# Optimization experiments

Hardware: AMD Instinct MI355X
Metric: run time of the kernel (lower is better)

## Reference

```python
import jax, jax.numpy as jnp
import numpy as np

GRID_SIZE = 10
SPLINE_ORDER = 3
GRID_RANGE = (0.0, 1.0)
COUNT_HARMONIC = 8


def make_grid():
    # knot vector: (grid_size + 2*spline_order + 1,) = (17,), same for every input feature
    h = (GRID_RANGE[1] - GRID_RANGE[0]) / GRID_SIZE
    return (jnp.arange(-SPLINE_ORDER, GRID_SIZE + SPLINE_ORDER + 1, dtype=jnp.float32) * h
            + GRID_RANGE[0])


def b_splines(x, grid):
    # x: (B, in) -> bases: (B, in, grid_size + spline_order) via Cox-de Boor recursion
    xg = x[..., None]                                   # (B, in, 1)
    bases = ((xg >= grid[:-1]) & (xg < grid[1:])).astype(x.dtype)  # (B, in, 16)
    for k in range(1, SPLINE_ORDER + 1):
        left = (xg - grid[:-(k + 1)]) / (grid[k:-1] - grid[:-(k + 1)]) * bases[..., :-1]
        right = (grid[k + 1:] - xg) / (grid[k + 1:] - grid[1:-k]) * bases[..., 1:]
        bases = left + right
    return bases                                        # (B, in, 13)


def kan_linear(x, base_w, spline_w, spline_scaler, grid):
    # base path: SiLU(x) @ W_base^T ; spline path: grouped weighted sum of B-spline bases
    base_out = jax.nn.silu(x) @ base_w.T                # (B, out)
    sp = b_splines(x, grid)                             # (B, in, C)
    sw = spline_w * spline_scaler[..., None]            # (out, in, C) standalone scaler
    spline_out = jnp.einsum('bic,oic->bo', sp, sw)
    return base_out + spline_out


def fft_calc(x):
    # x: (B, C, 64); two 32-sample windows, keep first count_harmonic+1 = 9 bins
    prev = jnp.fft.rfft(x[:, :, :32])[:, :, :COUNT_HARMONIC + 1]
    cur = jnp.fft.rfft(x[:, :, 32:])[:, :, :COUNT_HARMONIC + 1]
    # NOTE: original code uses the *current* window's phase twice (faithful to source)
    return jnp.concatenate(
        [jnp.abs(prev), jnp.angle(cur), jnp.abs(cur), jnp.angle(cur)], axis=-1)  # (B, C, 36)


def mlp_head(h, W1, b1, W2, b2, W3, b3):
    y = h @ W1.T + b1
    # nn.LeakyReLU(True) -> negative_slope = 1.0 -> identity (faithful to source)
    y = y @ W2.T + b2
    y = jnp.where(y >= 0, y, 0.05 * y)                  # LeakyReLU(0.05)
    y = y @ W3.T + b3
    return jax.nn.sigmoid(y)                            # (B, 1)


def setup_inputs() -> dict:
    key = jax.random.key(0)
    ks = jax.random.split(key, 20)
    B = 8192
    def n(i, shape):
        return jax.random.normal(ks[i], shape, dtype=jnp.float32)
    return {
        'x': n(0, (B, 64, 14)),
        'k1_base': n(1, (80, 504)), 'k1_spline': n(2, (80, 504, 13)), 'k1_scaler': n(3, (80, 504)),
        'k2_base': n(4, (160, 80)), 'k2_spline': n(5, (160, 80, 13)), 'k2_scaler': n(6, (160, 80)),
        'k3_base': n(7, (80, 160)), 'k3_spline': n(8, (80, 160, 13)), 'k3_scaler': n(9, (80, 160)),
        'k4_base': n(10, (40, 80)), 'k4_spline': n(11, (40, 80, 13)), 'k4_scaler': n(12, (40, 80)),
        'heads_W1': n(13, (3, 40, 40)), 'heads_b1': n(14, (3, 40)),
        'heads_W2': n(15, (3, 20, 40)), 'heads_b2': n(16, (3, 20)),
        'heads_W3': n(17, (3, 1, 20)), 'heads_b3': n(18, (3, 1)),
    }


def reference(x, k1_base, k1_spline, k1_scaler, k2_base, k2_spline, k2_scaler,
              k3_base, k3_spline, k3_scaler, k4_base, k4_spline, k4_scaler,
              heads_W1, heads_b1, heads_W2, heads_b2, heads_W3, heads_b3):
    B = x.shape[0]
    grid = make_grid()
    # original uses reshape (not transpose): (B, 64, 14) -> (B, 14, 64)
    h = x.reshape(B, x.shape[2], x.shape[1])
    h = fft_calc(h).reshape(B, -1)                      # (B, 504)
    h = kan_linear(h, k1_base, k1_spline, k1_scaler, grid)   # (B, 80)
    h = kan_linear(h, k2_base, k2_spline, k2_scaler, grid)   # (B, 160)
    h = kan_linear(h, k3_base, k3_spline, k3_scaler, grid)   # (B, 80)
    h = kan_linear(h, k4_base, k4_spline, k4_scaler, grid)   # (B, 40)
    heads = jax.vmap(lambda W1, b1, W2, b2, W3, b3: mlp_head(h, W1, b1, W2, b2, W3, b3))(
        heads_W1, heads_b1, heads_W2, heads_b2, heads_W3, heads_b3)  # (3, B, 1)
    return jnp.transpose(heads, (1, 0, 2)).reshape(B, 3)
```

## Files before the change

### kernel.cpp

```cpp
#include <hip/hip_runtime.h>
#include <math.h>


__device__ __forceinline__ float silu_f(float x) {
    return x / (1.f + __expf(-x));
}

__global__ __launch_bounds__(128) void fft_kernel(const float* __restrict__ x,
                                                  float* __restrict__ F0, int P) {
    __shared__ float xs[128 * 65];
    __shared__ float twc[288], tws[288];
    int tid = threadIdx.x;
    for (int t = tid; t < 288; t += 128) {
        int k = t >> 5, n = t & 31;
        int m = (k * n) & 31;
        float ang = -0.19634954084936207f * (float)m;
        float s, c;
        sincosf(ang, &s, &c);
        twc[t] = c; tws[t] = s;
    }
    int p0 = blockIdx.x * 128;
    for (int idx = tid; idx < 128 * 64; idx += 128) {
        int g = p0 * 64 + idx;
        float v = (g < P * 64) ? x[g] : 0.f;
        xs[(idx >> 6) * 65 + (idx & 63)] = v;
    }
    __syncthreads();
    int p = p0 + tid;
    if (p >= P) return;
    const float* row = &xs[tid * 65];
    float r[64];
#pragma unroll
    for (int n = 0; n < 64; ++n) r[n] = row[n];
    float outv[27];
#pragma unroll
    for (int k = 0; k < 9; ++k) {
        float rp = 0.f, ip = 0.f, rc = 0.f, ic = 0.f;
#pragma unroll
        for (int n = 0; n < 32; ++n) {
            float c = twc[k * 32 + n], s = tws[k * 32 + n];
            rp = fmaf(r[n], c, rp);
            ip = fmaf(r[n], s, ip);
            rc = fmaf(r[n + 32], c, rc);
            ic = fmaf(r[n + 32], s, ic);
        }
        float ap = sqrtf(fmaf(rp, rp, ip * ip));
        float ac = sqrtf(fmaf(rc, rc, ic * ic));
        float gc = atan2f(ic, rc);
        outv[k] = ap; outv[9 + k] = gc; outv[18 + k] = ac;
    }
    float* dst = &F0[(size_t)p * 27];
#pragma unroll
    for (int q = 0; q < 27; ++q) dst[q] = outv[q];
}

__global__ __launch_bounds__(256) void transpose_f0_kernel(const float* __restrict__ F0,
                                                           float* __restrict__ F0T, int B) {
    __shared__ float t[448 * 27];
    int b0 = blockIdx.x * 32;
    const float* src = F0 + (size_t)b0 * 14 * 27;
    for (int idx = threadIdx.x; idx < 448 * 27; idx += 256) t[idx] = src[idx];
    __syncthreads();
    for (int idx = threadIdx.x; idx < 378 * 32; idx += 256) {
        int i = idx >> 5, bb = idx & 31;
        int ch = i / 27, q = i - ch * 27;
        F0T[(size_t)i * B + b0 + bb] = t[(bb * 14 + ch) * 27 + q];
    }
}

__device__ __forceinline__ float kval(const float* __restrict__ bw,
                                      const float* __restrict__ sw,
                                      const float* __restrict__ sc,
                                      int IN, int o, int s, int c) {
    if (c == 0) return bw[o * IN + s];
    return sw[((size_t)o * IN + s) * 13 + (c - 1)] * sc[o * IN + s];
}

__global__ void prep_all_kernel(float* __restrict__ Wfp1, float* __restrict__ Wfp2,
                                float* __restrict__ Wfp3, float* __restrict__ Wfp4,
                                float* __restrict__ W21, float* __restrict__ b21,
                                const float* k1b, const float* k1s, const float* k1c,
                                const float* k2b, const float* k2s, const float* k2c,
                                const float* k3b, const float* k3s, const float* k3c,
                                const float* k4b, const float* k4s, const float* k4c,
                                const float* W1, const float* b1,
                                const float* W2, const float* b2) {
    const int T1 = 189 * 2688, T2 = 40 * 2 * 2688, T3 = 80 * 2688, T4 = 40 * 1344;
    int id = blockIdx.x * 256 + threadIdx.x;
    if (id < T1) {
        int jg = id / 2688, t = id % 2688;
        int kc = t / 96, t2 = t % 96, ct = t2 / 12, r = t2 % 12;
        int i = 2 * jg + kc / 14, c = kc % 14, o = ct * 10 + r;
        float v = 0.f;
        if (r < 10) {
            int ch = i / 27, q = i - ch * 27, s1 = ch * 36 + q;
            v = kval(k1b, k1s, k1c, 504, o, s1, c);
            if (q >= 9 && q < 18) v += kval(k1b, k1s, k1c, 504, o, s1 + 18, c);
        }
        Wfp1[id] = v; return;
    }
    id -= T1;
    if (id < T2) {
        int jg = id / (2 * 2688), rem = id % (2 * 2688), half = rem / 2688, t = rem % 2688;
        int kc = t / 96, t2 = t % 96, ct = t2 / 12, r = t2 % 12;
        int i = 2 * jg + kc / 14, c = kc % 14, o = half * 80 + ct * 10 + r;
        Wfp2[id] = (r < 10) ? kval(k2b, k2s, k2c, 80, o, i, c) : 0.f; return;
    }
    id -= T2;
    if (id < T3) {
        int jg = id / 2688, t = id % 2688;
        int kc = t / 96, t2 = t % 96, ct = t2 / 12, r = t2 % 12;
        int i = 2 * jg + kc / 14, c = kc % 14, o = ct * 10 + r;
        Wfp3[id] = (r < 10) ? kval(k3b, k3s, k3c, 160, o, i, c) : 0.f; return;
    }
    id -= T3;
    if (id < T4) {
        int jg = id / 1344, t = id % 1344;
        int kc = t / 48, t2 = t % 48, ct = t2 / 12, r = t2 % 12;
        int i = 2 * jg + kc / 14, c = kc % 14, o = ct * 10 + r;
        Wfp4[id] = (r < 10) ? kval(k4b, k4s, k4c, 80, o, i, c) : 0.f; return;
    }
    id -= T4;
    if (id < 3 * 20 * 40) {
        int k = id % 40, rem = id / 40, j = rem % 20, h = rem / 20;
        float a = 0.f;
        for (int m = 0; m < 40; ++m)
            a = fmaf(W2[(h * 20 + j) * 40 + m], W1[(h * 40 + m) * 40 + k], a);
        W21[id] = a;
    } else if (id < 3 * 20 * 40 + 60) {
        int t = id - 2400, j = t % 20, h = t / 20;
        float a = b2[h * 20 + j];
        for (int m = 0; m < 40; ++m)
            a = fmaf(W2[(h * 20 + j) * 40 + m], b1[h * 40 + m], a);
        b21[t] = a;
    }
}

template <int OUT_T, int KC, int NHALF>
__global__ __launch_bounds__(256) void kan5_kernel(const float* __restrict__ XT, int B,
                                                   const float* __restrict__ Wfp,
                                                   float* __restrict__ YpT, int OUTF) {
    constexpr int BM = 128;
    constexpr int NR = 10;
    constexpr int COLS_T = OUT_T / NR;
    constexpr int ROWS_T = 256 / COLS_T;
    constexpr int MR = BM / ROWS_T;
    constexpr int NW = 28 * COLS_T * 12;
    constexpr int NCH = KC / 2;
    constexpr int WSTG = (NW + 255) / 256;
    static_assert(COLS_T * NR == OUT_T, "cols");
    static_assert(ROWS_T * MR == BM, "rows");
    static_assert(KC % 2 == 0, "even KC");

    __shared__ float Ws[NW];
    __shared__ float Ft[28 * BM];

    const int tid = threadIdx.x;
    const int rt = tid % ROWS_T, ct = tid / ROWS_T;
    const int b0 = blockIdx.x * BM;
    const int s = blockIdx.y;
    const int half = blockIdx.z;
    const int ibase = s * KC;
    const int kk = tid >> 7;
    const int rr = tid & 127;

    float acc[MR][NR];
#pragma unroll
    for (int m = 0; m < MR; ++m)
#pragma unroll
        for (int n = 0; n < NR; ++n) acc[m][n] = 0.f;

    const size_t wbase0 = ((size_t)(ibase / 2) * NHALF + half) * NW;
    float wreg[WSTG];
#pragma unroll
    for (int u = 0; u < WSTG; ++u) {
        int t = tid + u * 256;
        wreg[u] = (t < NW) ? Wfp[wbase0 + t] : 0.f;
    }
    float xreg = XT[(size_t)(ibase + kk) * B + b0 + rr];

    for (int j = 0; j < NCH; ++j) {
        __syncthreads();
#pragma unroll
        for (int u = 0; u < WSTG; ++u) {
            int t = tid + u * 256;
            if (t < NW) Ws[t] = wreg[u];
        }
        {
            float xs = xreg;
            float* dst = &Ft[kk * 14 * BM + rr];
            dst[0] = silu_f(xs);
#pragma unroll
            for (int c = 1; c < 14; ++c) dst[c * BM] = 0.f;
            float t10 = (xs + 0.3f) * 10.f;
            if (t10 >= 0.f && t10 < 16.f) {
                int jj = (int)t10;
                float u = t10 - (float)jj;
                float u2 = u * u, u3 = u2 * u, v = 1.f - u;
                float B0 = v * v * v * (1.f / 6.f);
                float B1 = (3.f * u3 - 6.f * u2 + 4.f) * (1.f / 6.f);
                float B2 = (-3.f * u3 + 3.f * u2 + 3.f * u + 1.f) * (1.f / 6.f);
                float B3 = u3 * (1.f / 6.f);
                int bs = jj - 3;
#pragma unroll
                for (int t = 0; t < 4; ++t) {
                    int rw = bs + t;
                    float bb = (t == 0) ? B0 : (t == 1) ? B1 : (t == 2) ? B2 : B3;
                    if (rw >= 0 && rw <= 12) dst[(1 + rw) * BM] = bb;
                }
            }
        }
        if (j + 1 < NCH) {
            const size_t wb = wbase0 + (size_t)(j + 1) * NHALF * NW;
#pragma unroll
            for (int u = 0; u < WSTG; ++u) {
                int t = tid + u * 256;
                if (t < NW) wreg[u] = Wfp[wb + t];
            }
            xreg = XT[(size_t)(ibase + 2 * (j + 1) + kk) * B + b0 + rr];
        }
        __syncthreads();
#pragma unroll
        for (int kc = 0; kc < 28; ++kc) {
            const float* wb = &Ws[(kc * COLS_T + ct) * 12];
            float4 w0 = *(const float4*)(wb);
            float4 w1 = *(const float4*)(wb + 4);
            float2 w2 = *(const float2*)(wb + 8);
            float wn[NR] = {w0.x, w0.y, w0.z, w0.w, w1.x, w1.y, w1.z, w1.w, w2.x, w2.y};
            const float* fb = &Ft[kc * BM + rt * MR];
            float xm[MR];
            if constexpr (MR == 4) {
                float4 f = *(const float4*)fb;
                xm[0] = f.x; xm[1] = f.y; xm[2] = f.z; xm[3] = f.w;
            } else {
                float2 f = *(const float2*)fb;
                xm[0] = f.x; xm[1] = f.y;
            }
#pragma unroll
            for (int m = 0; m < MR; ++m)
#pragma unroll
                for (int n = 0; n < NR; ++n) acc[m][n] = fmaf(xm[m], wn[n], acc[m][n]);
        }
    }

    float* yd = YpT + (size_t)s * OUTF * B + (size_t)(half * OUT_T) * B;
#pragma unroll
    for (int n = 0; n < NR; ++n) {
        float* p = yd + (size_t)(ct * NR + n) * B + b0 + rt * MR;
        if constexpr (MR == 4)
            *(float4*)p = make_float4(acc[0][n], acc[1][n], acc[2][n], acc[3][n]);
        else
            *(float2*)p = make_float2(acc[0][n], acc[1][n]);
    }
}

__global__ void reduce_kernel(float* __restrict__ Y, const float* __restrict__ Yp,
                              int N, int KS) {
    int t = blockIdx.x * 256 + threadIdx.x;
    if (t >= N) return;
    float a = 0.f;
    for (int s = 0; s < KS; ++s) a += Yp[(size_t)s * N + t];
    Y[t] = a;
}

__global__ __launch_bounds__(256) void heads_kernel(const float* __restrict__ h4T,
                                                    const float* __restrict__ W21,
                                                    const float* __restrict__ b21,
                                                    const float* __restrict__ W3,
                                                    const float* __restrict__ b3,
                                                    float* __restrict__ out, int B) {
    __shared__ float w21s[2400], b21s[60], w3s[60], b3s[3];
    int tid = threadIdx.x;
    for (int t = tid; t < 2400; t += 256) w21s[t] = W21[t];
    if (tid < 60) { b21s[tid] = b21[tid]; w3s[tid] = W3[tid]; }
    if (tid < 3) b3s[tid] = b3[tid];
    __syncthreads();
    int id = blockIdx.x * 256 + tid;
    if (id >= B * 3) return;
    int b = id / 3, h = id % 3;
    float hv[40];
#pragma unroll
    for (int m = 0; m < 40; ++m) hv[m] = h4T[(size_t)m * B + b];
    float z = b3s[h];
#pragma unroll
    for (int j = 0; j < 20; ++j) {
        float y = b21s[h * 20 + j];
        const float* wr = &w21s[(h * 20 + j) * 40];
#pragma unroll
        for (int m = 0; m < 40; ++m) y = fmaf(wr[m], hv[m], y);
        y = (y >= 0.f) ? y : 0.05f * y;
        z = fmaf(w3s[h * 20 + j], y, z);
    }
    out[id] = 1.f / (1.f + __expf(-z));
}

extern "C" void kernel_launch(void* const* d_in, const int* in_sizes, int n_in,
                              void* d_out, int out_size, void* d_ws, size_t ws_size,
                              hipStream_t stream) {
    const float* x   = (const float*)d_in[0];
    const float* k1b = (const float*)d_in[1];
    const float* k1s = (const float*)d_in[2];
    const float* k1c = (const float*)d_in[3];
    const float* k2b = (const float*)d_in[4];
    const float* k2s = (const float*)d_in[5];
    const float* k2c = (const float*)d_in[6];
    const float* k3b = (const float*)d_in[7];
    const float* k3s = (const float*)d_in[8];
    const float* k3c = (const float*)d_in[9];
    const float* k4b = (const float*)d_in[10];
    const float* k4s = (const float*)d_in[11];
    const float* k4c = (const float*)d_in[12];
    const float* hW1 = (const float*)d_in[13];
    const float* hb1 = (const float*)d_in[14];
    const float* hW2 = (const float*)d_in[15];
    const float* hb2 = (const float*)d_in[16];
    const float* hW3 = (const float*)d_in[17];
    const float* hb3 = (const float*)d_in[18];
    float* out = (float*)d_out;

    int B = in_sizes[0] / (64 * 14);
    int P = B * 14;

    float* ws = (float*)d_ws;
    size_t off = 0;
    float* Wfp1 = ws + off; off += 189 * 2688;
    float* Wfp2 = ws + off; off += 40 * 2 * 2688;
    float* Wfp3 = ws + off; off += 80 * 2688;
    float* Wfp4 = ws + off; off += 40 * 1344;
    float* W21  = ws + off; off += 2400;
    float* b21  = ws + off; off += 60;
    float* F0T  = ws + off; off += (size_t)B * 378;
    float* h1T  = ws + off; off += (size_t)B * 80;
    float* h2T  = ws + off; off += (size_t)B * 160;
    float* h3T  = ws + off; off += (size_t)B * 80;
    float* h4T  = ws + off; off += (size_t)B * 40;
    float* F0   = ws + off;
    float* Yp   = ws + off;
    size_t cap = (ws_size / 4 > off) ? (ws_size / 4 - off) : 0;
    int S1 = (cap >= (size_t)21 * B * 80) ? 21 : (cap >= (size_t)9 * B * 80) ? 9
           : (cap >= (size_t)7 * B * 80) ? 7 : 3;
    int S2 = (cap >= (size_t)10 * B * 160) ? 10 : (cap >= (size_t)5 * B * 160) ? 5 : 2;
    int S3 = (cap >= (size_t)20 * B * 80) ? 20 : (cap >= (size_t)8 * B * 80) ? 8 : 4;
    int S4 = (cap >= (size_t)10 * B * 40) ? 10 : 2;

    {
        int total = 189 * 2688 + 40 * 2 * 2688 + 80 * 2688 + 40 * 1344 + 2460;
        prep_all_kernel<<<(total + 255) / 256, 256, 0, stream>>>(
            Wfp1, Wfp2, Wfp3, Wfp4, W21, b21,
            k1b, k1s, k1c, k2b, k2s, k2c, k3b, k3s, k3c, k4b, k4s, k4c,
            hW1, hb1, hW2, hb2);
    }

    fft_kernel<<<(P + 127) / 128, 128, 0, stream>>>(x, F0, P);
    transpose_f0_kernel<<<B / 32, 256, 0, stream>>>(F0, F0T, B);

    if (S1 == 21)     kan5_kernel<80, 18, 1><<<dim3(B / 128, 21, 1), 256, 0, stream>>>(F0T, B, Wfp1, Yp, 80);
    else if (S1 == 9) kan5_kernel<80, 42, 1><<<dim3(B / 128, 9, 1), 256, 0, stream>>>(F0T, B, Wfp1, Yp, 80);
    else if (S1 == 7) kan5_kernel<80, 54, 1><<<dim3(B / 128, 7, 1), 256, 0, stream>>>(F0T, B, Wfp1, Yp, 80);
    else              kan5_kernel<80, 126, 1><<<dim3(B / 128, 3, 1), 256, 0, stream>>>(F0T, B, Wfp1, Yp, 80);
    reduce_kernel<<<((B * 80) + 255) / 256, 256, 0, stream>>>(h1T, Yp, B * 80, S1);

    if (S2 == 10)     kan5_kernel<80, 8, 2><<<dim3(B / 128, 10, 2), 256, 0, stream>>>(h1T, B, Wfp2, Yp, 160);
    else if (S2 == 5) kan5_kernel<80, 16, 2><<<dim3(B / 128, 5, 2), 256, 0, stream>>>(h1T, B, Wfp2, Yp, 160);
    else              kan5_kernel<80, 40, 2><<<dim3(B / 128, 2, 2), 256, 0, stream>>>(h1T, B, Wfp2, Yp, 160);
    reduce_kernel<<<((B * 160) + 255) / 256, 256, 0, stream>>>(h2T, Yp, B * 160, S2);

    if (S3 == 20)     kan5_kernel<80, 8, 1><<<dim3(B / 128, 20, 1), 256, 0, stream>>>(h2T, B, Wfp3, Yp, 80);
    else if (S3 == 8) kan5_kernel<80, 20, 1><<<dim3(B / 128, 8, 1), 256, 0, stream>>>(h2T, B, Wfp3, Yp, 80);
    else              kan5_kernel<80, 40, 1><<<dim3(B / 128, 4, 1), 256, 0, stream>>>(h2T, B, Wfp3, Yp, 80);
    reduce_kernel<<<((B * 80) + 255) / 256, 256, 0, stream>>>(h3T, Yp, B * 80, S3);

    if (S4 == 10) kan5_kernel<40, 8, 1><<<dim3(B / 128, 10, 1), 256, 0, stream>>>(h3T, B, Wfp4, Yp, 40);
    else          kan5_kernel<40, 40, 1><<<dim3(B / 128, 2, 1), 256, 0, stream>>>(h3T, B, Wfp4, Yp, 40);
    reduce_kernel<<<((B * 40) + 255) / 256, 256, 0, stream>>>(h4T, Yp, B * 40, S4);

    heads_kernel<<<(B * 3 + 255) / 256, 256, 0, stream>>>(h4T, W21, b21, hW3, hb3, out, B);

    (void)n_in; (void)out_size;
}
```

Baseline: 389.2 us.

## Double-buffer KAN shared tiles, vectorize split-K reduce, retune split counts

```diff
diff --git a/kernel.cpp b/kernel.cpp
--- a/kernel.cpp
+++ b/kernel.cpp
@@ -137,7 +137,7 @@
 }
 
 template <int OUT_T, int KC, int NHALF>
-__global__ __launch_bounds__(256) void kan5_kernel(const float* __restrict__ XT, int B,
+__global__ __launch_bounds__(256) void kan6_kernel(const float* __restrict__ XT, int B,
                                                    const float* __restrict__ Wfp,
                                                    float* __restrict__ YpT, int OUTF) {
     constexpr int BM = 128;
@@ -152,8 +152,8 @@
     static_assert(ROWS_T * MR == BM, "rows");
     static_assert(KC % 2 == 0, "even KC");
 
-    __shared__ float Ws[NW];
-    __shared__ float Ft[28 * BM];
+    __shared__ float Ws[2][NW];
+    __shared__ float Ft[2][28 * BM];
 
     const int tid = threadIdx.x;
     const int rt = tid % ROWS_T, ct = tid / ROWS_T;
@@ -164,70 +164,76 @@
     const int kk = tid >> 7;
     const int rr = tid & 127;
 
+    const size_t wstride = (size_t)NHALF * NW;
+    const size_t wbase0 = ((size_t)(ibase / 2) * NHALF + half) * NW;
+
     float acc[MR][NR];
 #pragma unroll
     for (int m = 0; m < MR; ++m)
 #pragma unroll
         for (int n = 0; n < NR; ++n) acc[m][n] = 0.f;
 
-    const size_t wbase0 = ((size_t)(ibase / 2) * NHALF + half) * NW;
     float wreg[WSTG];
-#pragma unroll
-    for (int u = 0; u < WSTG; ++u) {
-        int t = tid + u * 256;
-        wreg[u] = (t < NW) ? Wfp[wbase0 + t] : 0.f;
-    }
-    float xreg = XT[(size_t)(ibase + kk) * B + b0 + rr];
-
-    for (int j = 0; j < NCH; ++j) {
-        __syncthreads();
+    float xreg;
+
+    auto loadw = [&](int jc) {
+        const float* src = Wfp + wbase0 + (size_t)jc * wstride;
 #pragma unroll
         for (int u = 0; u < WSTG; ++u) {
             int t = tid + u * 256;
-            if (t < NW) Ws[t] = wreg[u];
-        }
-        {
-            float xs = xreg;
-            float* dst = &Ft[kk * 14 * BM + rr];
-            dst[0] = silu_f(xs);
-#pragma unroll
-            for (int c = 1; c < 14; ++c) dst[c * BM] = 0.f;
-            float t10 = (xs + 0.3f) * 10.f;
-            if (t10 >= 0.f && t10 < 16.f) {
-                int jj = (int)t10;
-                float u = t10 - (float)jj;
-                float u2 = u * u, u3 = u2 * u, v = 1.f - u;
-                float B0 = v * v * v * (1.f / 6.f);
-                float B1 = (3.f * u3 - 6.f * u2 + 4.f) * (1.f / 6.f);
-                float B2 = (-3.f * u3 + 3.f * u2 + 3.f * u + 1.f) * (1.f / 6.f);
-                float B3 = u3 * (1.f / 6.f);
-                int bs = jj - 3;
-#pragma unroll
-                for (int t = 0; t < 4; ++t) {
-                    int rw = bs + t;
-                    float bb = (t == 0) ? B0 : (t == 1) ? B1 : (t == 2) ? B2 : B3;
-                    if (rw >= 0 && rw <= 12) dst[(1 + rw) * BM] = bb;
-                }
+            if (t < NW) wreg[u] = src[t];
+        }
+        xreg = XT[(size_t)(ibase + 2 * jc + kk) * B + b0 + rr];
+    };
+    auto commit = [&](int pb) {
+#pragma unroll
+        for (int u = 0; u < WSTG; ++u) {
+            int t = tid + u * 256;
+            if (t < NW) Ws[pb][t] = wreg[u];
+        }
+        float xs = xreg;
+        float* dst = &Ft[pb][kk * 14 * BM + rr];
+        dst[0] = silu_f(xs);
+#pragma unroll
+        for (int c = 1; c < 14; ++c) dst[c * BM] = 0.f;
+        float t10 = (xs + 0.3f) * 10.f;
+        if (t10 >= 0.f && t10 < 16.f) {
+            int jj = (int)t10;
+            float u = t10 - (float)jj;
+            float u2 = u * u, u3 = u2 * u, v = 1.f - u;
+            float B0 = v * v * v * (1.f / 6.f);
+            float B1 = (3.f * u3 - 6.f * u2 + 4.f) * (1.f / 6.f);
+            float B2 = (-3.f * u3 + 3.f * u2 + 3.f * u + 1.f) * (1.f / 6.f);
+            float B3 = u3 * (1.f / 6.f);
+            int bs = jj - 3;
+#pragma unroll
+            for (int t = 0; t < 4; ++t) {
+                int rw = bs + t;
+                float bb = (t == 0) ? B0 : (t == 1) ? B1 : (t == 2) ? B2 : B3;
+                if (rw >= 0 && rw <= 12) dst[(1 + rw) * BM] = bb;
             }
         }
+    };
+
+    loadw(0);
+    commit(0);
+    if (NCH > 1) loadw(1);
+    __syncthreads();
+
+    for (int j = 0; j < NCH; ++j) {
         if (j + 1 < NCH) {
-            const size_t wb = wbase0 + (size_t)(j + 1) * NHALF * NW;
-#pragma unroll
-            for (int u = 0; u < WSTG; ++u) {
-                int t = tid + u * 256;
-                if (t < NW) wreg[u] = Wfp[wb + t];
-            }
-            xreg = XT[(size_t)(ibase + 2 * (j + 1) + kk) * B + b0 + rr];
-        }
-        __syncthreads();
+            commit((j + 1) & 1);
+            if (j + 2 < NCH) loadw(j + 2);
+        }
+        const int pb = j & 1;
 #pragma unroll
         for (int kc = 0; kc < 28; ++kc) {
-            const float* wb = &Ws[(kc * COLS_T + ct) * 12];
+            const float* wb = &Ws[pb][(kc * COLS_T + ct) * 12];
             float4 w0 = *(const float4*)(wb);
             float4 w1 = *(const float4*)(wb + 4);
             float2 w2 = *(const float2*)(wb + 8);
             float wn[NR] = {w0.x, w0.y, w0.z, w0.w, w1.x, w1.y, w1.z, w1.w, w2.x, w2.y};
-            const float* fb = &Ft[kc * BM + rt * MR];
+            const float* fb = &Ft[pb][kc * BM + rt * MR];
             float xm[MR];
             if constexpr (MR == 4) {
                 float4 f = *(const float4*)fb;
@@ -241,6 +247,7 @@
 #pragma unroll
                 for (int n = 0; n < NR; ++n) acc[m][n] = fmaf(xm[m], wn[n], acc[m][n]);
         }
+        if (j + 1 < NCH) __syncthreads();
     }
 
     float* yd = YpT + (size_t)s * OUTF * B + (size_t)(half * OUT_T) * B;
@@ -257,10 +264,13 @@
 __global__ void reduce_kernel(float* __restrict__ Y, const float* __restrict__ Yp,
                               int N, int KS) {
     int t = blockIdx.x * 256 + threadIdx.x;
-    if (t >= N) return;
-    float a = 0.f;
-    for (int s = 0; s < KS; ++s) a += Yp[(size_t)s * N + t];
-    Y[t] = a;
+    if (t * 4 >= N) return;
+    float4 a = make_float4(0.f, 0.f, 0.f, 0.f);
+    for (int s = 0; s < KS; ++s) {
+        float4 v = *(const float4*)&Yp[(size_t)s * N + t * 4];
+        a.x += v.x; a.y += v.y; a.z += v.z; a.w += v.w;
+    }
+    *(float4*)&Y[t * 4] = a;
 }
 
 __global__ __launch_bounds__(256) void heads_kernel(const float* __restrict__ h4T,
@@ -337,11 +347,8 @@
     float* F0   = ws + off;
     float* Yp   = ws + off;
     size_t cap = (ws_size / 4 > off) ? (ws_size / 4 - off) : 0;
-    int S1 = (cap >= (size_t)21 * B * 80) ? 21 : (cap >= (size_t)9 * B * 80) ? 9
-           : (cap >= (size_t)7 * B * 80) ? 7 : 3;
-    int S2 = (cap >= (size_t)10 * B * 160) ? 10 : (cap >= (size_t)5 * B * 160) ? 5 : 2;
-    int S3 = (cap >= (size_t)20 * B * 80) ? 20 : (cap >= (size_t)8 * B * 80) ? 8 : 4;
-    int S4 = (cap >= (size_t)10 * B * 40) ? 10 : 2;
+
+    bool tierA = cap >= (size_t)800 * B;
 
     {
         int total = 189 * 2688 + 40 * 2 * 2688 + 80 * 2688 + 40 * 1344 + 2460;
@@ -354,25 +361,25 @@
     fft_kernel<<<(P + 127) / 128, 128, 0, stream>>>(x, F0, P);
     transpose_f0_kernel<<<B / 32, 256, 0, stream>>>(F0, F0T, B);
 
-    if (S1 == 21)     kan5_kernel<80, 18, 1><<<dim3(B / 128, 21, 1), 256, 0, stream>>>(F0T, B, Wfp1, Yp, 80);
-    else if (S1 == 9) kan5_kernel<80, 42, 1><<<dim3(B / 128, 9, 1), 256, 0, stream>>>(F0T, B, Wfp1, Yp, 80);
-    else if (S1 == 7) kan5_kernel<80, 54, 1><<<dim3(B / 128, 7, 1), 256, 0, stream>>>(F0T, B, Wfp1, Yp, 80);
-    else              kan5_kernel<80, 126, 1><<<dim3(B / 128, 3, 1), 256, 0, stream>>>(F0T, B, Wfp1, Yp, 80);
-    reduce_kernel<<<((B * 80) + 255) / 256, 256, 0, stream>>>(h1T, Yp, B * 80, S1);
-
-    if (S2 == 10)     kan5_kernel<80, 8, 2><<<dim3(B / 128, 10, 2), 256, 0, stream>>>(h1T, B, Wfp2, Yp, 160);
-    else if (S2 == 5) kan5_kernel<80, 16, 2><<<dim3(B / 128, 5, 2), 256, 0, stream>>>(h1T, B, Wfp2, Yp, 160);
-    else              kan5_kernel<80, 40, 2><<<dim3(B / 128, 2, 2), 256, 0, stream>>>(h1T, B, Wfp2, Yp, 160);
-    reduce_kernel<<<((B * 160) + 255) / 256, 256, 0, stream>>>(h2T, Yp, B * 160, S2);
-
-    if (S3 == 20)     kan5_kernel<80, 8, 1><<<dim3(B / 128, 20, 1), 256, 0, stream>>>(h2T, B, Wfp3, Yp, 80);
-    else if (S3 == 8) kan5_kernel<80, 20, 1><<<dim3(B / 128, 8, 1), 256, 0, stream>>>(h2T, B, Wfp3, Yp, 80);
-    else              kan5_kernel<80, 40, 1><<<dim3(B / 128, 4, 1), 256, 0, stream>>>(h2T, B, Wfp3, Yp, 80);
-    reduce_kernel<<<((B * 80) + 255) / 256, 256, 0, stream>>>(h3T, Yp, B * 80, S3);
-
-    if (S4 == 10) kan5_kernel<40, 8, 1><<<dim3(B / 128, 10, 1), 256, 0, stream>>>(h3T, B, Wfp4, Yp, 40);
-    else          kan5_kernel<40, 40, 1><<<dim3(B / 128, 2, 1), 256, 0, stream>>>(h3T, B, Wfp4, Yp, 40);
-    reduce_kernel<<<((B * 40) + 255) / 256, 256, 0, stream>>>(h4T, Yp, B * 40, S4);
+    if (tierA) {
+        kan6_kernel<80, 42, 1><<<dim3(B / 128, 9, 1), 256, 0, stream>>>(F0T, B, Wfp1, Yp, 80);
+        reduce_kernel<<<((B * 80 / 4) + 255) / 256, 256, 0, stream>>>(h1T, Yp, B * 80, 9);
+        kan6_kernel<80, 16, 2><<<dim3(B / 128, 5, 2), 256, 0, stream>>>(h1T, B, Wfp2, Yp, 160);
+        reduce_kernel<<<((B * 160 / 4) + 255) / 256, 256, 0, stream>>>(h2T, Yp, B * 160, 5);
+        kan6_kernel<80, 16, 1><<<dim3(B / 128, 10, 1), 256, 0, stream>>>(h2T, B, Wfp3, Yp, 80);
+        reduce_kernel<<<((B * 80 / 4) + 255) / 256, 256, 0, stream>>>(h3T, Yp, B * 80, 10);
+        kan6_kernel<40, 8, 1><<<dim3(B / 128, 10, 1), 256, 0, stream>>>(h3T, B, Wfp4, Yp, 40);
+        reduce_kernel<<<((B * 40 / 4) + 255) / 256, 256, 0, stream>>>(h4T, Yp, B * 40, 10);
+    } else {
+        kan6_kernel<80, 126, 1><<<dim3(B / 128, 3, 1), 256, 0, stream>>>(F0T, B, Wfp1, Yp, 80);
+        reduce_kernel<<<((B * 80 / 4) + 255) / 256, 256, 0, stream>>>(h1T, Yp, B * 80, 3);
+        kan6_kernel<80, 40, 2><<<dim3(B / 128, 2, 2), 256, 0, stream>>>(h1T, B, Wfp2, Yp, 160);
+        reduce_kernel<<<((B * 160 / 4) + 255) / 256, 256, 0, stream>>>(h2T, Yp, B * 160, 2);
+        kan6_kernel<80, 40, 1><<<dim3(B / 128, 4, 1), 256, 0, stream>>>(h2T, B, Wfp3, Yp, 80);
+        reduce_kernel<<<((B * 80 / 4) + 255) / 256, 256, 0, stream>>>(h3T, Yp, B * 80, 4);
+        kan6_kernel<40, 40, 1><<<dim3(B / 128, 2, 1), 256, 0, stream>>>(h3T, B, Wfp4, Yp, 40);
+        reduce_kernel<<<((B * 40 / 4) + 255) / 256, 256, 0, stream>>>(h4T, Yp, B * 40, 2);
+    }
 
     heads_kernel<<<(B * 3 + 255) / 256, 256, 0, stream>>>(h4T, W21, b21, hW3, hb3, out, B);
 
```

Result: slower. 428.3 us (+10.1%).
